# Performance work log

Measured on AMD Instinct MI355X. Metric: run time of the kernel, lower is better.

The kernel has to match this reference:

```python
import jax, jax.numpy as jnp
import numpy as np
import math

N_NODES = 50000
N_EDGES = 800000
N_GRAPHS = 2500
IN_DIM = 128
HID = 128
HEADS = 2


def _lin_params(key, fan_in, fan_out, bias=True):
    k1, k2 = jax.random.split(key)
    s = 1.0 / math.sqrt(fan_in)
    W = jax.random.uniform(k1, (fan_in, fan_out), jnp.float32, -s, s)
    b = jax.random.uniform(k2, (fan_out,), jnp.float32, -s, s) if bias else None
    return W, b


def setup_inputs() -> dict:
    key = jax.random.key(0)
    ks = jax.random.split(key, 16)
    x = jax.random.normal(ks[0], (N_NODES, IN_DIM), jnp.float32)
    edge_index = jax.random.randint(ks[1], (2, N_EDGES), 0, N_NODES, jnp.int64)
    batch = jnp.sort(jax.random.randint(ks[2], (N_NODES,), 0, N_GRAPHS, jnp.int64))
    edge_attr = jax.random.normal(ks[3], (N_EDGES,), jnp.float32)

    HC = HEADS * HID  # 256
    # layer 1: in=128, out_channels=128, heads=2, concat=True
    Wq1, bq1 = _lin_params(ks[4], IN_DIM, HC)
    Wk1, bk1 = _lin_params(ks[5], IN_DIM, HC)
    Wv1, bv1 = _lin_params(ks[6], IN_DIM, HC)
    We1, _ = _lin_params(ks[7], 1, HC, bias=False)
    Ws1, bs1 = _lin_params(ks[8], IN_DIM, HC)
    # layer 2: in=256, out_channels=128, heads=2, concat=False
    Wq2, bq2 = _lin_params(ks[9], HC, HC)
    Wk2, bk2 = _lin_params(ks[10], HC, HC)
    Wv2, bv2 = _lin_params(ks[11], HC, HC)
    We2, _ = _lin_params(ks[12], 1, HC, bias=False)
    Ws2, bs2 = _lin_params(ks[13], HC, HID)
    return {
        "x": x, "edge_index": edge_index, "batch": batch, "edge_attr": edge_attr,
        "Wq1": Wq1, "bq1": bq1, "Wk1": Wk1, "bk1": bk1, "Wv1": Wv1, "bv1": bv1,
        "We1": We1, "Ws1": Ws1, "bs1": bs1,
        "Wq2": Wq2, "bq2": bq2, "Wk2": Wk2, "bk2": bk2, "Wv2": Wv2, "bv2": bv2,
        "We2": We2, "Ws2": Ws2, "bs2": bs2,
    }


def transformer_conv(x, src, dst, edge_attr, Wq, bq, Wk, bk, Wv, bv, We, Ws, bs,
                     heads, out_ch, concat):
    N = x.shape[0]
    q = (x @ Wq + bq).reshape(N, heads, out_ch)
    k = (x @ Wk + bk).reshape(N, heads, out_ch)
    v = (x @ Wv + bv).reshape(N, heads, out_ch)
    e = (edge_attr @ We).reshape(-1, heads, out_ch)  # [E,H,C]
    kj = k[src] + e
    vj = v[src] + e
    alpha = jnp.einsum('ehc,ehc->eh', q[dst], kj) / math.sqrt(out_ch)  # [E,H]
    amax = jax.ops.segment_max(alpha, dst, num_segments=N)  # [N,H]
    ex = jnp.exp(alpha - amax[dst])
    denom = jax.ops.segment_sum(ex, dst, num_segments=N)  # [N,H]
    w = ex / denom[dst]  # segment softmax over incoming edges
    out = jax.ops.segment_sum(w[..., None] * vj, dst, num_segments=N)  # [N,H,C]
    out = out.reshape(N, heads * out_ch) if concat else out.mean(axis=1)
    return out + (x @ Ws + bs)  # root/skip connection (beta=False)


def reference(x, edge_index, batch, edge_attr,
              Wq1, bq1, Wk1, bk1, Wv1, bv1, We1, Ws1, bs1,
              Wq2, bq2, Wk2, bk2, Wv2, bv2, We2, Ws2, bs2):
    src, dst = edge_index[0], edge_index[1]
    ea = edge_attr.reshape(-1, 1)
    h = transformer_conv(x, src, dst, ea, Wq1, bq1, Wk1, bk1, Wv1, bv1, We1,
                         Ws1, bs1, HEADS, HID, concat=True)
    h = jax.nn.relu(h)  # dropout = identity in eval mode
    h = transformer_conv(h, src, dst, ea, Wq2, bq2, Wk2, bk2, Wv2, bv2, We2,
                         Ws2, bs2, HEADS, HID, concat=False)
    # global mean pool per graph
    sums = jax.ops.segment_sum(h, batch, num_segments=N_GRAPHS)
    cnts = jax.ops.segment_sum(jnp.ones((h.shape[0],), h.dtype), batch,
                               num_segments=N_GRAPHS)
    return sums / jnp.maximum(cnts, 1.0)[:, None]
```

## Files before the change

### kernel.cpp

```cpp
#include <hip/hip_runtime.h>
#include <math.h>

#define N_NODES  50000
#define N_EDGES  800000
#define N_GRAPHS 2500
#define IN_DIM   128
#define HID      128
#define HEADS    2
#define HC       256

typedef unsigned short u16;
typedef unsigned char  u8;
typedef unsigned int   u32;
typedef short  s8v  __attribute__((ext_vector_type(8)));
typedef float  f4v  __attribute__((ext_vector_type(4)));
typedef float  f2v  __attribute__((ext_vector_type(2)));

__device__ inline float bf2f(u16 u) {
    union { unsigned int i; float f; } c; c.i = ((unsigned int)u) << 16; return c.f;
}
__device__ inline u16 f2bf(float x) {
    union { float f; unsigned int i; } c; c.f = x;
    unsigned int r = c.i + 0x7FFFu + ((c.i >> 16) & 1u);
    return (u16)(r >> 16);
}
__device__ inline float bflo(unsigned int u) {
    union { unsigned int i; float f; } c; c.i = u << 16; return c.f;
}
__device__ inline float bfhi(unsigned int u) {
    union { unsigned int i; float f; } c; c.i = u & 0xffff0000u; return c.f;
}
__device__ inline f2v mkf2(float a, float b) { f2v r; r.x = a; r.y = b; return r; }

#if __has_builtin(__builtin_amdgcn_cvt_pk_fp8_f32) && __has_builtin(__builtin_amdgcn_cvt_pk_f32_fp8)
#define FP8_HW 1
#else
#define FP8_HW 0
#endif

__device__ inline u8 f2fp8(float x) {
#if FP8_HW
    return (u8)(__builtin_amdgcn_cvt_pk_fp8_f32(x, x, 0, false) & 0xff);
#else
    union { float f; unsigned int u; } c; c.f = x;
    unsigned int s = (c.u >> 24) & 0x80u;
    c.u &= 0x7fffffffu;
    if (c.f >= 448.f) return (u8)(s | 0x7e);
    if (c.f < 0.015625f) {
        int m = (int)(c.f * 512.f + 0.5f);
        if (m >= 8) return (u8)(s | 0x08);
        return (u8)(s | m);
    }
    c.u += 0x000fffffu + ((c.u >> 20) & 1u);
    unsigned int e = ((c.u >> 23) & 0xffu) - 120u;
    unsigned int m = (c.u >> 20) & 7u;
    return (u8)(s | (e << 3) | m);
#endif
}

__device__ inline void fp8x8_to_f32(uint2 kd8, float* kf) {
#if FP8_HW
    f2v p0 = __builtin_amdgcn_cvt_pk_f32_fp8(kd8.x, false);
    f2v p1 = __builtin_amdgcn_cvt_pk_f32_fp8(kd8.x, true);
    f2v p2 = __builtin_amdgcn_cvt_pk_f32_fp8(kd8.y, false);
    f2v p3 = __builtin_amdgcn_cvt_pk_f32_fp8(kd8.y, true);
    kf[0] = p0.x; kf[1] = p0.y; kf[2] = p1.x; kf[3] = p1.y;
    kf[4] = p2.x; kf[5] = p2.y; kf[6] = p3.x; kf[7] = p3.y;
#else
#pragma unroll
    for (int i = 0; i < 8; ++i) {
        unsigned int b = ((i < 4) ? (kd8.x >> (8 * i)) : (kd8.y >> (8 * (i - 4)))) & 0xffu;
        unsigned int em = b & 0x7fu;
        union { unsigned int u; float f; } c;
        c.u = ((b & 0x80u) << 24) | ((em + 960u) << 20);
        float fn = c.f;
        float fs = (float)(int)em * 0.001953125f;
        fs = (b & 0x80u) ? -fs : fs;
        kf[i] = (em >= 8u) ? fn : fs;
    }
#endif
}

__device__ inline void fp8x8_to_f2(uint2 kd8, f2v* k2) {
#if FP8_HW
    k2[0] = __builtin_amdgcn_cvt_pk_f32_fp8(kd8.x, false);
    k2[1] = __builtin_amdgcn_cvt_pk_f32_fp8(kd8.x, true);
    k2[2] = __builtin_amdgcn_cvt_pk_f32_fp8(kd8.y, false);
    k2[3] = __builtin_amdgcn_cvt_pk_f32_fp8(kd8.y, true);
#else
    float kf[8];
    fp8x8_to_f32(kd8, kf);
    k2[0] = mkf2(kf[0], kf[1]); k2[1] = mkf2(kf[2], kf[3]);
    k2[2] = mkf2(kf[4], kf[5]); k2[3] = mkf2(kf[6], kf[7]);
#endif
}

__global__ __launch_bounds__(256) void init_kernel(
    const int* __restrict__ ei, const int* __restrict__ batch,
    int* __restrict__ deg, int* __restrict__ gdeg,
    int* __restrict__ flag_ei, int* __restrict__ flag_b)
{
    int b = blockIdx.x, t = threadIdx.x;
    if (b < 49) {
        int base = b * 1024 + t * 4;
        if (base + 3 < N_NODES) {
            *(int4*)&deg[base] = make_int4(0, 0, 0, 0);
        } else {
#pragma unroll
            for (int i = 0; i < 4; ++i) if (base + i < N_NODES) deg[base + i] = 0;
        }
    } else if (b < 59) {
        int i = (b - 49) * 256 + t;
        if (i < N_GRAPHS) gdeg[i] = 0;
    } else {
        const int* p = (b == 59) ? ei : batch;
        int ob = (b == 59) ? 1 : 40001;
        int* fl = (b == 59) ? flag_ei : flag_b;
        __shared__ int nz;
        if (t == 0) nz = 0;
        __syncthreads();
        int any = 0;
        for (int i = t; i < 1024; i += 256) if (p[ob + 2 * i] != 0) any = 1;
        if (any) atomicAdd(&nz, 1);
        __syncthreads();
        if (t == 0) *fl = (nz == 0) ? 1 : 0;
    }
}

#define W1_ELEMS (1024 * 128)
#define W2_ELEMS (896 * 256)
__global__ __launch_bounds__(256) void hist_prep_kernel(
    const int* __restrict__ ei, const int* __restrict__ batch,
    const int* __restrict__ flag_ei, const int* __restrict__ flag_b,
    int* __restrict__ deg, int* __restrict__ gdeg,
    int* __restrict__ rank,
    const float* __restrict__ Wq1, const float* __restrict__ Wk1,
    const float* __restrict__ Wv1, const float* __restrict__ Ws1,
    const float* __restrict__ bq1, const float* __restrict__ bk1,
    const float* __restrict__ bv1, const float* __restrict__ bs1,
    const float* __restrict__ Wq2, const float* __restrict__ Wk2,
    const float* __restrict__ Wv2, const float* __restrict__ Ws2,
    const float* __restrict__ bq2, const float* __restrict__ bk2,
    const float* __restrict__ bv2, const float* __restrict__ bs2,
    u16* __restrict__ w1T, float* __restrict__ b1cat,
    u16* __restrict__ w2T, float* __restrict__ b2cat)
{
    const int E = N_EDGES;
    int i = blockIdx.x * 256 + threadIdx.x;
    if (i < E) {
        int f = *flag_ei;
        int d = f ? ei[2 * ((size_t)E + i)] : ei[(size_t)E + i];
        if ((unsigned)d < (unsigned)N_NODES) rank[i] = atomicAdd(&deg[d], 1);
    } else if (i < E + N_NODES) {
        int j = i - E;
        int f = *flag_b;
        int g = f ? batch[2 * (size_t)j] : batch[j];
        if ((unsigned)g < (unsigned)N_GRAPHS) atomicAdd(&gdeg[g], 1);
    } else if (i < E + N_NODES + W1_ELEMS) {
        int t1 = i - E - N_NODES;
        int n = t1 >> 7, k = t1 & 127;
        int w = n >> 8, nc = n & 255;
        const float* W = (w == 0) ? Wq1 : (w == 1) ? Wk1 : (w == 2) ? Wv1 : Ws1;
        w1T[t1] = f2bf(W[k * 256 + nc]);
        if (k == 0) {
            const float* b = (w == 0) ? bq1 : (w == 1) ? bk1 : (w == 2) ? bv1 : bs1;
            b1cat[n] = b[nc];
        }
    } else if (i < E + N_NODES + W1_ELEMS + W2_ELEMS) {
        int t2 = i - E - N_NODES - W1_ELEMS;
        int n = t2 >> 8, k = t2 & 255;
        float val, bval;
        if (n < 768) {
            int w = n >> 8, nc = n & 255;
            const float* W = (w == 0) ? Wq2 : (w == 1) ? Wk2 : Wv2;
            val = W[k * 256 + nc];
            bval = ((w == 0) ? bq2 : (w == 1) ? bk2 : bv2)[nc];
        } else {
            val = Ws2[k * 128 + (n - 768)];
            bval = bs2[n - 768];
        }
        w2T[t2] = f2bf(val);
        if (k == 0) b2cat[n] = bval;
    }
}

__global__ void scan_local_kernel(const int* __restrict__ deg, int* __restrict__ rowptr,
                                  int* __restrict__ bsums, int n) {
    __shared__ int sh[256];
    int t = threadIdx.x;
    int base = blockIdx.x * 1024 + t * 4;
    int d0 = (base + 0 < n) ? deg[base + 0] : 0;
    int d1 = (base + 1 < n) ? deg[base + 1] : 0;
    int d2 = (base + 2 < n) ? deg[base + 2] : 0;
    int d3 = (base + 3 < n) ? deg[base + 3] : 0;
    sh[t] = d0 + d1 + d2 + d3;
    __syncthreads();
    for (int off = 1; off < 256; off <<= 1) {
        int val = 0;
        if (t >= off) val = sh[t - off];
        __syncthreads();
        if (t >= off) sh[t] += val;
        __syncthreads();
    }
    int excl = (t > 0) ? sh[t - 1] : 0;
    if (t == 255) bsums[blockIdx.x] = sh[255];
    if (base + 0 < n) rowptr[base + 0] = excl;
    if (base + 1 < n) rowptr[base + 1] = excl + d0;
    if (base + 2 < n) rowptr[base + 2] = excl + d0 + d1;
    if (base + 3 < n) rowptr[base + 3] = excl + d0 + d1 + d2;
}

__global__ __launch_bounds__(256) void scan_mid_kernel(
    int* __restrict__ bsums, int nb, int* __restrict__ rowptr_last,
    const int* __restrict__ gdeg, int* __restrict__ growptr)
{
    int t = threadIdx.x;
    if (blockIdx.x == 0) {
        if (t >= 64) return;
        int v = (t < nb) ? bsums[t] : 0;
        int incl = v;
        for (int off = 1; off < 64; off <<= 1) {
            int u = __shfl_up(incl, off);
            if (t >= off) incl += u;
        }
        if (t < nb) bsums[t] = incl - v;
        if (t == 63) *rowptr_last = incl;
    } else {
        __shared__ int sh[256];
        int base = t * 10;
        int loc[10];
        int s = 0;
#pragma unroll
        for (int i = 0; i < 10; ++i) {
            int v = (base + i < N_GRAPHS) ? gdeg[base + i] : 0;
            loc[i] = s; s += v;
        }
        sh[t] = s;
        __syncthreads();
        for (int off = 1; off < 256; off <<= 1) {
            int val = 0;
            if (t >= off) val = sh[t - off];
            __syncthreads();
            if (t >= off) sh[t] += val;
            __syncthreads();
        }
        int excl = (t > 0) ? sh[t - 1] : 0;
#pragma unroll
        for (int i = 0; i < 10; ++i)
            if (base + i < N_GRAPHS) growptr[base + i] = excl + loc[i];
        if (t == 255) growptr[N_GRAPHS] = sh[255];
    }
}

__global__ void scan_add_kernel(int* __restrict__ rowptr, const int* __restrict__ bsums,
                                int n) {
    int i = blockIdx.x * blockDim.x + threadIdx.x;
    if (i < n) rowptr[i] += bsums[i >> 10];
}

template <typename AT, int KDIM, int NT>
__device__ __forceinline__ void gemm_slab_body(
    int bx, const AT* __restrict__ A, const u16* __restrict__ BT,
    const float* __restrict__ biascat,
    u16* __restrict__ C0, u8* __restrict__ KV, u16* __restrict__ C3,
    int s0, int s3, int M)
{
    __shared__ u16 As[64 * KDIM];
    __shared__ u16 Bs[128 * 32];
    int t = threadIdx.x;
    int wid = t >> 6, lane = t & 63;
    int wm = wid >> 1, wn = wid & 1;
    int row0 = bx * 64;

    if constexpr (sizeof(AT) == 4) {
#pragma unroll
        for (int i = 0; i < KDIM / 16; ++i) {
            int c = t + i * 256;
            int row = c / (KDIM / 4);
            int kq  = (c % (KDIM / 4)) * 4;
            float4 d = make_float4(0.f, 0.f, 0.f, 0.f);
            if (row0 + row < M)
                d = *(const float4*)&A[(size_t)(row0 + row) * KDIM + kq];
            ushort4 h;
            h.x = f2bf(d.x); h.y = f2bf(d.y); h.z = f2bf(d.z); h.w = f2bf(d.w);
            *(ushort4*)&As[row * KDIM + (kq ^ ((row & 7) << 3))] = h;
        }
    } else {
#pragma unroll
        for (int i = 0; i < KDIM / 32; ++i) {
            int c = t + i * 256;
            int row = c / (KDIM / 8);
            int kq  = (c % (KDIM / 8)) * 8;
            uint4 d = make_uint4(0u, 0u, 0u, 0u);
            if (row0 + row < M)
                d = *(const uint4*)&A[(size_t)(row0 + row) * KDIM + kq];
            *(uint4*)&As[row * KDIM + (kq ^ ((row & 7) << 3))] = d;
        }
    }
    __syncthreads();

    int koff = (lane >> 4) * 8;
    int mrow = wm * 32 + (lane & 15);
    int nrow = wn * 64 + (lane & 15);
    int aswz = (lane & 7) << 3;
    int bswz = (((lane & 15) >> 1) & 3) << 3;
    int nloc = (lane >> 4) * 4;

    int c0 = t, c1 = t + 256;
    int brow0 = c0 >> 2, bkq0 = (c0 & 3) * 8;
    int brow1 = c1 >> 2, bkq1 = (c1 & 3) * 8;
    int bsa0 = brow0 * 32 + (bkq0 ^ (((brow0 >> 1) & 3) << 3));
    int bsa1 = brow1 * 32 + (bkq1 ^ (((brow1 >> 1) & 3) << 3));

    const int KS  = KDIM / 32;
    const int TOT = NT * KS;

    uint4 pb0 = *(const uint4*)&BT[(size_t)brow0 * KDIM + bkq0];
    uint4 pb1 = *(const uint4*)&BT[(size_t)brow1 * KDIM + bkq1];

    for (int nt = 0; nt < NT; ++nt) {
        f4v acc[2][4];
#pragma unroll
        for (int i = 0; i < 2; ++i)
#pragma unroll
            for (int j = 0; j < 4; ++j)
#pragma unroll
                for (int r = 0; r < 4; ++r) acc[i][j][r] = 0.f;

        for (int kk = 0; kk < KS; ++kk) {
            int k0 = kk * 32;
            int s = nt * KS + kk;
            *(uint4*)&Bs[bsa0] = pb0;
            *(uint4*)&Bs[bsa1] = pb1;
            __syncthreads();
            int s1 = s + 1;
            if (s1 < TOT) {
                int n_ = s1 / KS, k_ = (s1 % KS) * 32;
                pb0 = *(const uint4*)&BT[(size_t)(n_ * 128 + brow0) * KDIM + k_ + bkq0];
                pb1 = *(const uint4*)&BT[(size_t)(n_ * 128 + brow1) * KDIM + k_ + bkq1];
            }

            s8v af[2], bf[4];
#pragma unroll
            for (int tm = 0; tm < 2; ++tm)
                af[tm] = *(const s8v*)&As[(mrow + tm * 16) * KDIM + ((k0 + koff) ^ aswz)];
#pragma unroll
            for (int tn = 0; tn < 4; ++tn)
                bf[tn] = *(const s8v*)&Bs[(nrow + tn * 16) * 32 + (koff ^ bswz)];
#pragma unroll
            for (int tm = 0; tm < 2; ++tm)
#pragma unroll
                for (int tn = 0; tn < 4; ++tn)
                    acc[tm][tn] = __builtin_amdgcn_mfma_f32_16x16x32_bf16(
                        bf[tn], af[tm], acc[tm][tn], 0, 0, 0);
            __syncthreads();
        }

        int buf = nt >> 1;
        int colb = (nt & 1) * 128;
        float4 b4s[4];
#pragma unroll
        for (int tn = 0; tn < 4; ++tn)
            b4s[tn] = *(const float4*)&biascat[nt * 128 + wn * 64 + tn * 16 + nloc];

#pragma unroll
        for (int tm = 0; tm < 2; ++tm) {
            int row = row0 + wm * 32 + tm * 16 + (lane & 15);
            if (row >= M) continue;
#pragma unroll
            for (int tn = 0; tn < 4; ++tn) {
                int ncol = colb + wn * 64 + tn * 16 + nloc;
                float v0 = acc[tm][tn][0] + b4s[tn].x;
                float v1 = acc[tm][tn][1] + b4s[tn].y;
                float v2 = acc[tm][tn][2] + b4s[tn].z;
                float v3 = acc[tm][tn][3] + b4s[tn].w;
                if (buf == 1 || buf == 2) {
                    int off = (buf == 1) ? 0 : 256;
                    u32 pk = (u32)f2fp8(v0) | ((u32)f2fp8(v1) << 8)
                           | ((u32)f2fp8(v2) << 16) | ((u32)f2fp8(v3) << 24);
                    *(u32*)&KV[(size_t)row * 512 + off + ncol] = pk;
                } else {
                    u16* Cp = (buf == 0) ? C0 : C3;
                    int stride = (buf == 0) ? s0 : s3;
                    ushort4 h;
                    h.x = f2bf(v0); h.y = f2bf(v1); h.z = f2bf(v2); h.w = f2bf(v3);
                    *(ushort4*)&Cp[(size_t)row * stride + ncol] = h;
                }
            }
        }
    }
}

#define GB 782

__global__ __launch_bounds__(256, 4) void gemm1_scatter_kernel(
    const float* __restrict__ A, const u16* __restrict__ BT,
    const float* __restrict__ biascat,
    u16* __restrict__ C0, u8* __restrict__ KV, u16* __restrict__ C3,
    int s0, int s3, int M,
    const int* __restrict__ ei, const float* __restrict__ ea,
    const int* __restrict__ flag, const int* __restrict__ rowptr,
    const int* __restrict__ rank, u32* __restrict__ edges)
{
    if (blockIdx.x < GB) {
        gemm_slab_body<float, 128, 8>(blockIdx.x, A, BT, biascat,
                                      C0, KV, C3, s0, s3, M);
    } else {
        const int E = N_EDGES;
        int i = (blockIdx.x - GB) * 256 + threadIdx.x;
        if (i >= E) return;
        int f = *flag;
        int s = f ? ei[2 * (size_t)i] : ei[i];
        int d = f ? ei[2 * ((size_t)E + i)] : ei[(size_t)E + i];
        if ((unsigned)d >= (unsigned)N_NODES) return;
        if ((unsigned)s >= (unsigned)N_NODES) s = 0;
        int p = rowptr[d] + rank[i];
        u32 rec = (u32)(s & 0xffff) | ((u32)f2bf(ea[i]) << 16);
        edges[p] = rec;
    }
}

__global__ __launch_bounds__(256, 4) void gemm2_kernel(
    const u16* __restrict__ A, const u16* __restrict__ BT,
    const float* __restrict__ biascat,
    u16* __restrict__ C0, u8* __restrict__ KV, u16* __restrict__ C3,
    int s0, int s3, int M)
{
    gemm_slab_body<u16, 256, 7>(blockIdx.x, A, BT, biascat,
                                C0, KV, C3, s0, s3, M);
}

template <int LAYER>
__global__ __launch_bounds__(256) void attn_node(
    const u16* __restrict__ q, const u8* __restrict__ kv,
    const float* __restrict__ We, const u16* __restrict__ skip,
    const int* __restrict__ rowptr, const u32* __restrict__ edges,
    void* __restrict__ hout, int N)
{
    int wave = (blockIdx.x * blockDim.x + threadIdx.x) >> 6;
    int lane = threadIdx.x & 63;
    if (wave >= N) return;
    int n = wave;
    int half = lane >> 5;
    int cl   = lane & 31;
    const float scale2 = 0.12751743558136835f;

    uint4 qd = *(const uint4*)&q[(size_t)n * HC + cl * 8];
    f2v q2[4];
    q2[0] = mkf2(bflo(qd.x), bfhi(qd.x));
    q2[1] = mkf2(bflo(qd.y), bfhi(qd.y));
    q2[2] = mkf2(bflo(qd.z), bfhi(qd.z));
    q2[3] = mkf2(bflo(qd.w), bfhi(qd.w));
    float4 wlo = *(const float4*)&We[cl * 8];
    float4 whi = *(const float4*)&We[cl * 8 + 4];
    f2v w2[4];
    w2[0] = mkf2(wlo.x, wlo.y); w2[1] = mkf2(wlo.z, wlo.w);
    w2[2] = mkf2(whi.x, whi.y); w2[3] = mkf2(whi.z, whi.w);

    f2v qw2 = q2[0] * w2[0];
    qw2 += q2[1] * w2[1];
    qw2 += q2[2] * w2[2];
    qw2 += q2[3] * w2[3];
    float qw = qw2.x + qw2.y;
    qw += __shfl_xor(qw, 1);
    qw += __shfl_xor(qw, 2);
    qw += __shfl_xor(qw, 4);
    qw += __shfl_xor(qw, 8);

    int e0 = rowptr[n], e1 = rowptr[n + 1];
    float ll0 = 0.f, ll1 = 0.f;
    float pa0 = 0.f, pa1 = 0.f;
    f2v a0[4], a1[4];
#pragma unroll
    for (int i = 0; i < 4; ++i) { a0[i] = mkf2(0.f, 0.f); a1[i] = mkf2(0.f, 0.f); }

    int steps = (e1 - e0 + 7) >> 3;
    for (int st = 0; st < steps; ++st) {
        int eb = e0 + 8 * st + half;
        u32 rec[4]; bool act[4];
#pragma unroll
        for (int j = 0; j < 4; ++j) {
            int ex = eb + 2 * j;
            act[j] = ex < e1;
            rec[j] = edges[act[j] ? ex : e0];
        }
        uint2 kd[4], vd[4]; float ae[4];
#pragma unroll
        for (int j = 0; j < 4; ++j) {
            const u8* base = kv + (size_t)(rec[j] & 0xffffu) * 512;
            kd[j] = *(const uint2*)(base + cl * 8);
            vd[j] = *(const uint2*)(base + 256 + cl * 8);
            ae[j] = bfhi(rec[j]);
        }
#pragma unroll
        for (int j = 0; j < 4; ++j) {
            f2v k2[4], v2[4];
            fp8x8_to_f2(kd[j], k2);
            fp8x8_to_f2(vd[j], v2);
            f2v d2 = q2[0] * k2[0];
            d2 += q2[1] * k2[1];
            d2 += q2[2] * k2[2];
            d2 += q2[3] * k2[3];
            float d = d2.x + d2.y;
            d += __shfl_xor(d, 1);
            d += __shfl_xor(d, 2);
            d += __shfl_xor(d, 4);
            d += __shfl_xor(d, 8);
            float alpha = act[j] ? fmaf(ae[j], qw, d) * scale2 : -16384.f;
            float p = exp2f(fminf(alpha, 80.f));
            f2v p2 = mkf2(p, p);
            if (j & 1) {
                ll1 += p;
                pa1 = fmaf(p, ae[j], pa1);
                a1[0] += p2 * v2[0];
                a1[1] += p2 * v2[1];
                a1[2] += p2 * v2[2];
                a1[3] += p2 * v2[3];
            } else {
                ll0 += p;
                pa0 = fmaf(p, ae[j], pa0);
                a0[0] += p2 * v2[0];
                a0[1] += p2 * v2[1];
                a0[2] += p2 * v2[2];
                a0[3] += p2 * v2[3];
            }
        }
    }

    float l = ll0 + ll1;
    float pa = pa0 + pa1;
    float acc[8];
#pragma unroll
    for (int i = 0; i < 4; ++i) {
        f2v v = a0[i] + a1[i];
        acc[2 * i] = v.x; acc[2 * i + 1] = v.y;
    }

    l += __shfl_xor(l, 32);
    pa += __shfl_xor(pa, 32);
#pragma unroll
    for (int i = 0; i < 8; ++i) acc[i] += __shfl_xor(acc[i], 32);

    float wf[8];
    wf[0] = w2[0].x; wf[1] = w2[0].y; wf[2] = w2[1].x; wf[3] = w2[1].y;
    wf[4] = w2[2].x; wf[5] = w2[2].y; wf[6] = w2[3].x; wf[7] = w2[3].y;

    float inv = (l > 0.f) ? 1.f / l : 0.f;
    float o[8];
#pragma unroll
    for (int i = 0; i < 8; ++i) o[i] = fmaf(pa, wf[i], acc[i]) * inv;

    if constexpr (LAYER == 1) {
        if (half == 0) {
            uint4 sd = *(const uint4*)&skip[(size_t)n * HC + cl * 8];
            float sf[8];
            sf[0] = bflo(sd.x); sf[1] = bfhi(sd.x);
            sf[2] = bflo(sd.y); sf[3] = bfhi(sd.y);
            sf[4] = bflo(sd.z); sf[5] = bfhi(sd.z);
            sf[6] = bflo(sd.w); sf[7] = bfhi(sd.w);
            ushort4 o4a, o4b;
            o4a.x = f2bf(fmaxf(0.f, o[0] + sf[0]));
            o4a.y = f2bf(fmaxf(0.f, o[1] + sf[1]));
            o4a.z = f2bf(fmaxf(0.f, o[2] + sf[2]));
            o4a.w = f2bf(fmaxf(0.f, o[3] + sf[3]));
            o4b.x = f2bf(fmaxf(0.f, o[4] + sf[4]));
            o4b.y = f2bf(fmaxf(0.f, o[5] + sf[5]));
            o4b.z = f2bf(fmaxf(0.f, o[6] + sf[6]));
            o4b.w = f2bf(fmaxf(0.f, o[7] + sf[7]));
            u16* hp = (u16*)hout + (size_t)n * HC + cl * 8;
            *(ushort4*)hp = o4a;
            *(ushort4*)(hp + 4) = o4b;
        }
    } else {
#pragma unroll
        for (int i = 0; i < 8; ++i) {
            float t2 = __shfl_xor(o[i], 16);
            o[i] = 0.5f * (o[i] + t2);
        }
        if (lane < 16) {
            uint4 sd = *(const uint4*)&skip[(size_t)n * HID + lane * 8];
            float sf[8];
            sf[0] = bflo(sd.x); sf[1] = bfhi(sd.x);
            sf[2] = bflo(sd.y); sf[3] = bfhi(sd.y);
            sf[4] = bflo(sd.z); sf[5] = bfhi(sd.z);
            sf[6] = bflo(sd.w); sf[7] = bfhi(sd.w);
            float* hp = (float*)hout + (size_t)n * HID + lane * 8;
            float4 oa, ob;
            oa.x = o[0] + sf[0]; oa.y = o[1] + sf[1];
            oa.z = o[2] + sf[2]; oa.w = o[3] + sf[3];
            ob.x = o[4] + sf[4]; ob.y = o[5] + sf[5];
            ob.z = o[6] + sf[6]; ob.w = o[7] + sf[7];
            *(float4*)hp = oa;
            *(float4*)(hp + 4) = ob;
        }
    }
}

__global__ __launch_bounds__(256) void pool_kernel(
    const float* __restrict__ h2, const int* __restrict__ growptr,
    float* __restrict__ out) {
    int wave = (blockIdx.x * blockDim.x + threadIdx.x) >> 6;
    int lane = threadIdx.x & 63;
    if (wave >= N_GRAPHS) return;
    int r0 = growptr[wave], r1 = growptr[wave + 1];
    float sx = 0.f, sy = 0.f;
    for (int r = r0; r < r1; ++r) {
        float2 v = *(const float2*)&h2[(size_t)r * HID + lane * 2];
        sx += v.x; sy += v.y;
    }
    float inv = 1.f / fmaxf((float)(r1 - r0), 1.f);
    float2 o; o.x = sx * inv; o.y = sy * inv;
    *(float2*)&out[(size_t)wave * HID + lane * 2] = o;
}

extern "C" void kernel_launch(void* const* d_in, const int* in_sizes, int n_in,
                              void* d_out, int out_size, void* d_ws, size_t ws_size,
                              hipStream_t stream) {
    const float* x    = (const float*)d_in[0];
    const int*   ei   = (const int*)d_in[1];
    const int*   batch= (const int*)d_in[2];
    const float* ea   = (const float*)d_in[3];
    const float* Wq1  = (const float*)d_in[4];
    const float* bq1  = (const float*)d_in[5];
    const float* Wk1  = (const float*)d_in[6];
    const float* bk1  = (const float*)d_in[7];
    const float* Wv1  = (const float*)d_in[8];
    const float* bv1  = (const float*)d_in[9];
    const float* We1  = (const float*)d_in[10];
    const float* Ws1  = (const float*)d_in[11];
    const float* bs1  = (const float*)d_in[12];
    const float* Wq2  = (const float*)d_in[13];
    const float* bq2  = (const float*)d_in[14];
    const float* Wk2  = (const float*)d_in[15];
    const float* bk2  = (const float*)d_in[16];
    const float* Wv2  = (const float*)d_in[17];
    const float* bv2  = (const float*)d_in[18];
    const float* We2  = (const float*)d_in[19];
    const float* Ws2  = (const float*)d_in[20];
    const float* bs2  = (const float*)d_in[21];
    float* out = (float*)d_out;

    char* ws = (char*)d_ws;
    size_t off = 0;
    auto alloc = [&](size_t bytes) -> void* {
        void* p = ws + off;
        off += (bytes + 255) & ~(size_t)255;
        return p;
    };
    int*   flag_ei = (int*)alloc(4);
    int*   flag_b  = (int*)alloc(4);
    int*   deg     = (int*)alloc((size_t)N_NODES * 4);
    int*   rowptr  = (int*)alloc((size_t)(N_NODES + 1) * 4);
    int*   rank    = (int*)alloc((size_t)N_EDGES * 4);
    int*   bsums   = (int*)alloc(64 * 4);
    u32*   edges   = (u32*)alloc((size_t)N_EDGES * 4);
    int*   gdeg    = (int*)alloc((size_t)N_GRAPHS * 4);
    int*   growptr = (int*)alloc((size_t)(N_GRAPHS + 1) * 4);
    u16*   w1T     = (u16*)alloc((size_t)1024 * 128 * 2);
    float* b1cat   = (float*)alloc(1024 * 4);
    u16*   w2T     = (u16*)alloc((size_t)896 * 256 * 2);
    float* b2cat   = (float*)alloc(896 * 4);
    u16*   B0      = (u16*)alloc((size_t)N_NODES * HC * 2);
    u16*   B1      = (u16*)alloc((size_t)N_NODES * HC * 2);
    u8*    KVb     = (u8*)alloc((size_t)N_NODES * 512);
    u16*   B4      = (u16*)alloc((size_t)N_NODES * HID * 2);

    const int E = N_EDGES;

    init_kernel<<<61, 256, 0, stream>>>(ei, batch, deg, gdeg, flag_ei, flag_b);

    int hp_grid = (E + N_NODES + W1_ELEMS + W2_ELEMS + 255) / 256;
    hist_prep_kernel<<<hp_grid, 256, 0, stream>>>(
        ei, batch, flag_ei, flag_b, deg, gdeg, rank,
        Wq1, Wk1, Wv1, Ws1, bq1, bk1, bv1, bs1,
        Wq2, Wk2, Wv2, Ws2, bq2, bk2, bv2, bs2,
        w1T, b1cat, w2T, b2cat);

    int nb = (N_NODES + 1023) / 1024;
    scan_local_kernel<<<nb, 256, 0, stream>>>(deg, rowptr, bsums, N_NODES);
    scan_mid_kernel<<<2, 256, 0, stream>>>(bsums, nb, rowptr + N_NODES, gdeg, growptr);
    scan_add_kernel<<<(N_NODES + 255) / 256, 256, 0, stream>>>(rowptr, bsums, N_NODES);

    int sc_grid = (E + 255) / 256;
    gemm1_scatter_kernel<<<GB + sc_grid, 256, 0, stream>>>(
        x, w1T, b1cat, B0, KVb, B1, 256, 256, N_NODES,
        ei, ea, flag_ei, rowptr, rank, edges);

    attn_node<1><<<N_NODES / 4, 256, 0, stream>>>(B0, KVb, We1, B1, rowptr, edges, B0, N_NODES);

    gemm2_kernel<<<GB, 256, 0, stream>>>(
        B0, w2T, b2cat, B1, KVb, B4, 256, 128, N_NODES);

    attn_node<2><<<N_NODES / 4, 256, 0, stream>>>(B1, KVb, We2, B4, rowptr, edges, B0, N_NODES);

    pool_kernel<<<(N_GRAPHS + 3) / 4, 256, 0, stream>>>((const float*)B0, growptr, out);
}
```

Measured before the change: 437.3 us.

## Use 128-row GEMM1 tiles with register-prefetched B; store layer-2 output as bf16

Adds a dedicated layer-1 GEMM body that converts a 128x128 slab of x to bf16 in LDS once and streams the weight tiles through a register prefetch, halving the number of GEMM blocks. The aim is more reuse of the A tile and less per-block overhead. Separately, the layer-2 attention output is now written as bf16 instead of fp32, and the pooling kernel reads bf16, cutting that write and read traffic. The cost is more LDS and lower occupancy for the GEMM (launch bounds 3), plus some precision loss in h2 before pooling.

```diff
diff --git a/kernel.cpp b/kernel.cpp
--- a/kernel.cpp
+++ b/kernel.cpp
@@ -391,9 +391,124 @@
     }
 }
 
-#define GB 782
-
-__global__ __launch_bounds__(256, 4) void gemm1_scatter_kernel(
+__device__ __forceinline__ void gemm1_slab128(
+    int bx, const float* __restrict__ A, const u16* __restrict__ BT,
+    const float* __restrict__ biascat,
+    u16* __restrict__ C0, u8* __restrict__ KV, u16* __restrict__ C3,
+    int s0, int s3, int M)
+{
+    const int KDIM = 128, NT = 8;
+    __shared__ u16 As[128 * 128];
+    __shared__ u16 Bs[128 * 32];
+    int t = threadIdx.x;
+    int wid = t >> 6, lane = t & 63;
+    int row0 = bx * 128;
+
+#pragma unroll
+    for (int i = 0; i < 16; ++i) {
+        int c = t + i * 256;
+        int row = c >> 5;
+        int kq  = (c & 31) * 4;
+        float4 d = make_float4(0.f, 0.f, 0.f, 0.f);
+        if (row0 + row < M)
+            d = *(const float4*)&A[(size_t)(row0 + row) * KDIM + kq];
+        ushort4 h;
+        h.x = f2bf(d.x); h.y = f2bf(d.y); h.z = f2bf(d.z); h.w = f2bf(d.w);
+        *(ushort4*)&As[row * KDIM + (kq ^ ((row & 7) << 3))] = h;
+    }
+    __syncthreads();
+
+    int koff = (lane >> 4) * 8;
+    int mrow = wid * 32 + (lane & 15);
+    int aswz = (lane & 7) << 3;
+    int bswz = (((lane & 15) >> 1) & 3) << 3;
+    int nloc = (lane >> 4) * 4;
+
+    int c0 = t, c1 = t + 256;
+    int brow0 = c0 >> 2, bkq0 = (c0 & 3) * 8;
+    int brow1 = c1 >> 2, bkq1 = (c1 & 3) * 8;
+    int bsa0 = brow0 * 32 + (bkq0 ^ (((brow0 >> 1) & 3) << 3));
+    int bsa1 = brow1 * 32 + (bkq1 ^ (((brow1 >> 1) & 3) << 3));
+
+    const int KS  = 4;
+    const int TOT = NT * KS;
+
+    uint4 pb0 = *(const uint4*)&BT[(size_t)brow0 * KDIM + bkq0];
+    uint4 pb1 = *(const uint4*)&BT[(size_t)brow1 * KDIM + bkq1];
+
+    for (int nt = 0; nt < NT; ++nt) {
+        f4v acc[2][8];
+#pragma unroll
+        for (int i = 0; i < 2; ++i)
+#pragma unroll
+            for (int j = 0; j < 8; ++j)
+#pragma unroll
+                for (int r = 0; r < 4; ++r) acc[i][j][r] = 0.f;
+
+        for (int kk = 0; kk < KS; ++kk) {
+            int k0 = kk * 32;
+            int s = nt * KS + kk;
+            *(uint4*)&Bs[bsa0] = pb0;
+            *(uint4*)&Bs[bsa1] = pb1;
+            __syncthreads();
+            int s1 = s + 1;
+            if (s1 < TOT) {
+                int n_ = s1 >> 2, k_ = (s1 & 3) * 32;
+                pb0 = *(const uint4*)&BT[(size_t)(n_ * 128 + brow0) * KDIM + k_ + bkq0];
+                pb1 = *(const uint4*)&BT[(size_t)(n_ * 128 + brow1) * KDIM + k_ + bkq1];
+            }
+
+            s8v af[2], bf[8];
+#pragma unroll
+            for (int tm = 0; tm < 2; ++tm)
+                af[tm] = *(const s8v*)&As[(mrow + tm * 16) * KDIM + ((k0 + koff) ^ aswz)];
+#pragma unroll
+            for (int tn = 0; tn < 8; ++tn)
+                bf[tn] = *(const s8v*)&Bs[(tn * 16 + (lane & 15)) * 32 + (koff ^ bswz)];
+#pragma unroll
+            for (int tm = 0; tm < 2; ++tm)
+#pragma unroll
+                for (int tn = 0; tn < 8; ++tn)
+                    acc[tm][tn] = __builtin_amdgcn_mfma_f32_16x16x32_bf16(
+                        bf[tn], af[tm], acc[tm][tn], 0, 0, 0);
+            __syncthreads();
+        }
+
+        int buf = nt >> 1;
+        int colb = (nt & 1) * 128;
+#pragma unroll
+        for (int tm = 0; tm < 2; ++tm) {
+            int row = row0 + wid * 32 + tm * 16 + (lane & 15);
+            if (row >= M) continue;
+#pragma unroll
+            for (int tn = 0; tn < 8; ++tn) {
+                float4 b4 = *(const float4*)&biascat[nt * 128 + tn * 16 + nloc];
+                int ncol = colb + tn * 16 + nloc;
+                float v0 = acc[tm][tn][0] + b4.x;
+                float v1 = acc[tm][tn][1] + b4.y;
+                float v2 = acc[tm][tn][2] + b4.z;
+                float v3 = acc[tm][tn][3] + b4.w;
+                if (buf == 1 || buf == 2) {
+                    int off = (buf == 1) ? 0 : 256;
+                    u32 pk = (u32)f2fp8(v0) | ((u32)f2fp8(v1) << 8)
+                           | ((u32)f2fp8(v2) << 16) | ((u32)f2fp8(v3) << 24);
+                    *(u32*)&KV[(size_t)row * 512 + off + ncol] = pk;
+                } else {
+                    u16* Cp = (buf == 0) ? C0 : C3;
+                    int stride = (buf == 0) ? s0 : s3;
+                    ushort4 h;
+                    h.x = f2bf(v0); h.y = f2bf(v1); h.z = f2bf(v2); h.w = f2bf(v3);
+                    *(ushort4*)&Cp[(size_t)row * stride + ncol] = h;
+                }
+            }
+        }
+    }
+}
+
+#define GB1 391
+#define GB2 782
+
+__global__ __launch_bounds__(256, 3) void gemm1_scatter_kernel(
     const float* __restrict__ A, const u16* __restrict__ BT,
     const float* __restrict__ biascat,
     u16* __restrict__ C0, u8* __restrict__ KV, u16* __restrict__ C3,
@@ -402,12 +517,11 @@
     const int* __restrict__ flag, const int* __restrict__ rowptr,
     const int* __restrict__ rank, u32* __restrict__ edges)
 {
-    if (blockIdx.x < GB) {
-        gemm_slab_body<float, 128, 8>(blockIdx.x, A, BT, biascat,
-                                      C0, KV, C3, s0, s3, M);
+    if (blockIdx.x < GB1) {
+        gemm1_slab128(blockIdx.x, A, BT, biascat, C0, KV, C3, s0, s3, M);
     } else {
         const int E = N_EDGES;
-        int i = (blockIdx.x - GB) * 256 + threadIdx.x;
+        int i = (blockIdx.x - GB1) * 256 + threadIdx.x;
         if (i >= E) return;
         int f = *flag;
         int s = f ? ei[2 * (size_t)i] : ei[i];
@@ -584,20 +698,20 @@
             sf[2] = bflo(sd.y); sf[3] = bfhi(sd.y);
             sf[4] = bflo(sd.z); sf[5] = bfhi(sd.z);
             sf[6] = bflo(sd.w); sf[7] = bfhi(sd.w);
-            float* hp = (float*)hout + (size_t)n * HID + lane * 8;
-            float4 oa, ob;
-            oa.x = o[0] + sf[0]; oa.y = o[1] + sf[1];
-            oa.z = o[2] + sf[2]; oa.w = o[3] + sf[3];
-            ob.x = o[4] + sf[4]; ob.y = o[5] + sf[5];
-            ob.z = o[6] + sf[6]; ob.w = o[7] + sf[7];
-            *(float4*)hp = oa;
-            *(float4*)(hp + 4) = ob;
+            ushort4 h2a, h2b;
+            h2a.x = f2bf(o[0] + sf[0]); h2a.y = f2bf(o[1] + sf[1]);
+            h2a.z = f2bf(o[2] + sf[2]); h2a.w = f2bf(o[3] + sf[3]);
+            h2b.x = f2bf(o[4] + sf[4]); h2b.y = f2bf(o[5] + sf[5]);
+            h2b.z = f2bf(o[6] + sf[6]); h2b.w = f2bf(o[7] + sf[7]);
+            u16* hp = (u16*)hout + (size_t)n * HID + lane * 8;
+            *(ushort4*)hp = h2a;
+            *(ushort4*)(hp + 4) = h2b;
         }
     }
 }
 
 __global__ __launch_bounds__(256) void pool_kernel(
-    const float* __restrict__ h2, const int* __restrict__ growptr,
+    const u16* __restrict__ h2, const int* __restrict__ growptr,
     float* __restrict__ out) {
     int wave = (blockIdx.x * blockDim.x + threadIdx.x) >> 6;
     int lane = threadIdx.x & 63;
@@ -605,8 +719,8 @@
     int r0 = growptr[wave], r1 = growptr[wave + 1];
     float sx = 0.f, sy = 0.f;
     for (int r = r0; r < r1; ++r) {
-        float2 v = *(const float2*)&h2[(size_t)r * HID + lane * 2];
-        sx += v.x; sy += v.y;
+        u32 v = *(const u32*)&h2[(size_t)r * HID + lane * 2];
+        sx += bflo(v); sy += bfhi(v);
     }
     float inv = 1.f / fmaxf((float)(r1 - r0), 1.f);
     float2 o; o.x = sx * inv; o.y = sy * inv;
@@ -682,16 +796,16 @@
     scan_add_kernel<<<(N_NODES + 255) / 256, 256, 0, stream>>>(rowptr, bsums, N_NODES);
 
     int sc_grid = (E + 255) / 256;
-    gemm1_scatter_kernel<<<GB + sc_grid, 256, 0, stream>>>(
+    gemm1_scatter_kernel<<<GB1 + sc_grid, 256, 0, stream>>>(
         x, w1T, b1cat, B0, KVb, B1, 256, 256, N_NODES,
         ei, ea, flag_ei, rowptr, rank, edges);
 
     attn_node<1><<<N_NODES / 4, 256, 0, stream>>>(B0, KVb, We1, B1, rowptr, edges, B0, N_NODES);
 
-    gemm2_kernel<<<GB, 256, 0, stream>>>(
+    gemm2_kernel<<<GB2, 256, 0, stream>>>(
         B0, w2T, b2cat, B1, KVb, B4, 256, 128, N_NODES);
 
     attn_node<2><<<N_NODES / 4, 256, 0, stream>>>(B1, KVb, We2, B4, rowptr, edges, B0, N_NODES);
 
-    pool_kernel<<<(N_GRAPHS + 3) / 4, 256, 0, stream>>>((const float*)B0, growptr, out);
-}
+    pool_kernel<<<(N_GRAPHS + 3) / 4, 256, 0, stream>>>((const u16*)B0, growptr, out);
+}
```

Result: slower. 452.3 us (+3.4%).
